# Performance work log

Hardware: AMD Instinct MI355X
Metric: run time of the kernel (lower is better)

## Reference

```python
import jax, jax.numpy as jnp
import numpy as np

EPS = 1e-15
B, N, F, K = 16, 1024, 512, 128  # graphs, max_nodes, feat dim, clusters


def setup_inputs() -> dict:
    key = jax.random.key(0)
    k0, k1, k2 = jax.random.split(key, 3)
    rng = np.random.default_rng(0)
    # Ragged graph sizes (between N/2 and N nodes per graph)
    counts = rng.integers(N // 2, N + 1, size=B)
    T = int(counts.sum())
    batch = np.repeat(np.arange(B), counts)
    starts = np.repeat(np.concatenate([[0], np.cumsum(counts)[:-1]]), counts)
    column = np.arange(T) - starts
    flat_index = batch * N + column  # as in _build_motifpool_dense_layout
    mask_flat = np.zeros(B * N, dtype=bool)
    mask_flat[flat_index] = True
    mask = mask_flat.reshape(B, N)
    x = jax.random.normal(k0, (T, F), dtype=jnp.float32)
    s = jax.random.normal(k1, (T, K), dtype=jnp.float32)
    a = jax.random.uniform(k2, (B, N, N), dtype=jnp.float32)
    m = jnp.asarray(mask)
    adj = (a + a.transpose(0, 2, 1)) * m[:, :, None] * m[:, None, :]
    return {
        'x': x,
        's': s,
        'adj': adj,
        'flat_index': jnp.asarray(flat_index, dtype=jnp.int32),
        'mask': m,
    }


def reference(x, s, adj, flat_index, mask):
    Bn, Nn = mask.shape
    Fd = x.shape[-1]
    Kd = s.shape[-1]
    # ragged -> dense scatter (index_copy_ equivalent)
    xd = jnp.zeros((Bn * Nn, Fd), x.dtype).at[flat_index].set(x).reshape(Bn, Nn, Fd)
    sd = jnp.zeros((Bn * Nn, Kd), s.dtype).at[flat_index].set(s).reshape(Bn, Nn, Kd)
    fmask = mask[..., None].astype(x.dtype)  # [B,N,1]
    sm = jax.nn.softmax(sd, axis=-1) * fmask
    xm = xd * fmask
    # pooled features and adjacency
    out = jnp.einsum('bnk,bnf->bkf', sm, xm)
    sa = jnp.einsum('bnk,bnm->bkm', sm, adj)
    out_adj = jnp.einsum('bkm,bml->bkl', sa, sm)
    # mincut loss: tr(S^T A S) / tr(S^T D S)
    mincut_num = jnp.trace(out_adj, axis1=-2, axis2=-1)
    d_flat = adj.sum(-1)  # node degrees [B,N]
    mincut_den = jnp.einsum('bn,bnk,bnk->b', d_flat, sm, sm)
    mincut_loss = jnp.mean(-(mincut_num / mincut_den))
    # orthogonality loss
    ss = jnp.einsum('bnk,bnl->bkl', sm, sm)
    ss_norm = jnp.linalg.norm(ss, axis=(-2, -1), keepdims=True)
    i_s = jnp.eye(Kd, dtype=ss.dtype)
    ortho_loss = jnp.mean(
        jnp.linalg.norm(ss / ss_norm - i_s / jnp.sqrt(jnp.asarray(Kd, ss.dtype)),
                        axis=(-2, -1)))
    # zero diagonal, symmetric degree-normalize
    eye_b = jnp.eye(Kd, dtype=bool)
    out_adj = jnp.where(eye_b, jnp.zeros((), out_adj.dtype), out_adj)
    d = jnp.sqrt(out_adj.sum(-1))[:, None, :] + EPS  # [B,1,K]
    out_adj = out_adj / d / d.transpose(0, 2, 1)
    return (sm, out, out_adj, mincut_loss, ortho_loss)
```

## Files before the change

kernel.cpp:

```cpp
#include <hip/hip_runtime.h>

constexpr int NB = 16, NN = 1024, NF = 512, NK = 128;
constexpr int NCH = 8;
constexpr int MSPLIT = 2;
constexpr float EPSV = 1e-15f;

typedef __attribute__((ext_vector_type(8))) short bf16x8;
typedef __attribute__((ext_vector_type(4))) float f32x4;

__device__ __forceinline__ f32x4 MFMA(bf16x8 a, bf16x8 b, f32x4 c) {
  return __builtin_amdgcn_mfma_f32_16x16x32_bf16(a, b, c, 0, 0, 0);
}

__device__ __forceinline__ unsigned short bf16_rn(float f) {
  unsigned int u = __float_as_uint(f);
  u += 0x7fffu + ((u >> 16) & 1u);
  return (unsigned short)(u >> 16);
}
__device__ __forceinline__ float bf16f(unsigned short h) {
  return __uint_as_float((unsigned int)h << 16);
}
__device__ __forceinline__ void split2(float f, unsigned short& h, unsigned short& lo) {
  h = bf16_rn(f);
  lo = bf16_rn(f - bf16f(h));
}

__global__ __launch_bounds__(256) void k_softmax(const float* __restrict__ s,
                                                 const int* __restrict__ fidx, int T,
                                                 float* __restrict__ sm,
                                                 unsigned short* __restrict__ smTh,
                                                 unsigned short* __restrict__ smTl,
                                                 int* __restrict__ rowof) {
  __shared__ float P[64][129];
  __shared__ int rof[64];
  int blk = blockIdx.x;
  int b = blk >> 4, n0 = (blk & 15) * 64;
  int tid = threadIdx.x, wv = tid >> 6, lane = tid & 63;
  if (tid < 64) {
    int d = b * NN + n0 + tid;
    int lo = 0, hi = T;
    while (lo < hi) {
      int mid = (lo + hi) >> 1;
      if (fidx[mid] < d) lo = mid + 1; else hi = mid;
    }
    int r = (lo < T && fidx[lo] == d) ? lo : -1;
    rof[tid] = r;
    rowof[d] = r;
  }
  __syncthreads();
  for (int i = 0; i < 16; ++i) {
    int r = wv * 16 + i;
    int ri = rof[r];
    float e0 = 0.f, e1 = 0.f;
    if (ri >= 0) {
      const float* row = s + (size_t)ri * NK;
      float a = row[lane], c = row[lane + 64];
      float m = fmaxf(a, c);
#pragma unroll
      for (int off = 32; off; off >>= 1) m = fmaxf(m, __shfl_xor(m, off, 64));
      e0 = expf(a - m);
      e1 = expf(c - m);
      float sum = e0 + e1;
#pragma unroll
      for (int off = 32; off; off >>= 1) sum += __shfl_xor(sum, off, 64);
      float inv = 1.0f / sum;
      e0 *= inv;
      e1 *= inv;
    }
    P[r][lane] = e0;
    P[r][lane + 64] = e1;
  }
  __syncthreads();
  int r2 = tid >> 2, cb = (tid & 3) * 32;
  float* orow = sm + ((size_t)b * NN + n0 + r2) * NK + cb;
#pragma unroll
  for (int j = 0; j < 8; ++j) {
    float4 v = make_float4(P[r2][cb + j * 4], P[r2][cb + j * 4 + 1],
                           P[r2][cb + j * 4 + 2], P[r2][cb + j * 4 + 3]);
    *(float4*)(orow + j * 4) = v;
  }
  for (int j = 0; j < 32; ++j) {
    int k = wv * 32 + j;
    float v = P[lane][k];
    unsigned short h, lo;
    split2(v, h, lo);
    size_t off = ((size_t)b * NK + k) * NN + n0 + lane;
    smTh[off] = h;
    smTl[off] = lo;
  }
}

__global__ __launch_bounds__(256) void k_adj_sm(const float* __restrict__ adj,
                                                const unsigned short* __restrict__ smTh,
                                                const unsigned short* __restrict__ smTl,
                                                float* __restrict__ Ytp,
                                                float* __restrict__ dfp) {
  __shared__ __align__(16) unsigned short STh[128][72], STl[128][72];
  __shared__ __align__(16) unsigned short ADh[64][72], ADl[64][72];
  int b = blockIdx.y, n0 = blockIdx.x * 64, z = blockIdx.z;
  int tid = threadIdx.x, wv = tid >> 6, l = tid & 63;
  int lr = l & 15, lk = l >> 4;
  int tk = tid >> 1, th = tid & 1;
  int sn = tid >> 2, sq = tid & 3;
  const float* A = adj + (size_t)b * NN * NN;
  f32x4 zero = {0.f, 0.f, 0.f, 0.f};
  f32x4 acc[2][4];
#pragma unroll
  for (int i = 0; i < 2; ++i)
#pragma unroll
    for (int j = 0; j < 4; ++j) acc[i][j] = zero;
  float rsacc = 0.f;
  for (int m0 = z * (NN / MSPLIT); m0 < (z + 1) * (NN / MSPLIT); m0 += 64) {
    __syncthreads();
    {
      const uint4* gh = (const uint4*)(smTh + ((size_t)b * NK + tk) * NN + m0 + th * 32);
      const uint4* gl = (const uint4*)(smTl + ((size_t)b * NK + tk) * NN + m0 + th * 32);
#pragma unroll
      for (int j = 0; j < 4; ++j) {
        *(uint4*)&STh[tk][th * 32 + j * 8] = gh[j];
        *(uint4*)&STl[tk][th * 32 + j * 8] = gl[j];
      }
    }
    {
      const float* ap = A + (size_t)(n0 + sn) * NN + m0 + sq * 16;
      float ps = 0.f;
#pragma unroll
      for (int j = 0; j < 4; ++j) {
        float4 v = *(const float4*)(ap + j * 4);
        ushort4 vh, vl;
        split2(v.x, vh.x, vl.x);
        split2(v.y, vh.y, vl.y);
        split2(v.z, vh.z, vl.z);
        split2(v.w, vh.w, vl.w);
        *(ushort4*)&ADh[sn][sq * 16 + j * 4] = vh;
        *(ushort4*)&ADl[sn][sq * 16 + j * 4] = vl;
        ps += v.x + v.y + v.z + v.w;
      }
      ps += __shfl_xor(ps, 1, 64);
      ps += __shfl_xor(ps, 2, 64);
      rsacc += ps;
    }
    __syncthreads();
#pragma unroll
    for (int s = 0; s < 2; ++s) {
      bf16x8 ah0 = *(const bf16x8*)&STh[wv * 32 + lr][s * 32 + lk * 8];
      bf16x8 ah1 = *(const bf16x8*)&STh[wv * 32 + 16 + lr][s * 32 + lk * 8];
      bf16x8 al0 = *(const bf16x8*)&STl[wv * 32 + lr][s * 32 + lk * 8];
      bf16x8 al1 = *(const bf16x8*)&STl[wv * 32 + 16 + lr][s * 32 + lk * 8];
#pragma unroll
      for (int nt = 0; nt < 4; ++nt) {
        bf16x8 bh = *(const bf16x8*)&ADh[nt * 16 + lr][s * 32 + lk * 8];
        bf16x8 bl = *(const bf16x8*)&ADl[nt * 16 + lr][s * 32 + lk * 8];
        acc[0][nt] = MFMA(ah0, bh, acc[0][nt]);
        acc[0][nt] = MFMA(ah0, bl, acc[0][nt]);
        acc[0][nt] = MFMA(al0, bh, acc[0][nt]);
        acc[1][nt] = MFMA(ah1, bh, acc[1][nt]);
        acc[1][nt] = MFMA(ah1, bl, acc[1][nt]);
        acc[1][nt] = MFMA(al1, bh, acc[1][nt]);
      }
    }
  }
  float* Yb = Ytp + ((size_t)z * NB + b) * NK * NN;
#pragma unroll
  for (int kt = 0; kt < 2; ++kt)
#pragma unroll
    for (int nt = 0; nt < 4; ++nt)
#pragma unroll
      for (int reg = 0; reg < 4; ++reg) {
        int k = wv * 32 + kt * 16 + lk * 4 + reg;
        int n = n0 + nt * 16 + lr;
        Yb[(size_t)k * NN + n] = acc[kt][nt][reg];
      }
  if (sq == 0) dfp[((size_t)z * NB + b) * NN + n0 + sn] = rsacc;
}

__global__ __launch_bounds__(512) void k_feat(const unsigned short* __restrict__ smTh,
                                              const unsigned short* __restrict__ smTl,
                                              const float* __restrict__ x,
                                              const int* __restrict__ rowof,
                                              float* __restrict__ outf) {
  __shared__ __align__(16) unsigned short STh[64][72], STl[64][72];
  __shared__ __align__(16) unsigned short XTh[64][72], XTl[64][72];
  int b = blockIdx.y, fbase = blockIdx.x * 64, kh = blockIdx.z * 64;
  int tid = threadIdx.x, wv = tid >> 6, l = tid & 63;
  int lr = l & 15, lk = l >> 4;
  int wk = (wv >> 1) * 16, wf = (wv & 1) * 32;
  int tk = tid >> 3, tq = tid & 7;
  f32x4 zero = {0.f, 0.f, 0.f, 0.f};
  f32x4 acc[2] = {zero, zero};
  for (int n0 = 0; n0 < NN; n0 += 64) {
    __syncthreads();
    {
      const uint4* gh = (const uint4*)(smTh + ((size_t)b * NK + kh + tk) * NN + n0 + tq * 8);
      const uint4* gl = (const uint4*)(smTl + ((size_t)b * NK + kh + tk) * NN + n0 + tq * 8);
      *(uint4*)&STh[tk][tq * 8] = gh[0];
      *(uint4*)&STl[tk][tq * 8] = gl[0];
    }
    {
      int ri = rowof[b * NN + n0 + tk];
      if (ri >= 0) {
        const float* xp = x + (size_t)ri * NF + fbase + tq * 8;
#pragma unroll
        for (int j = 0; j < 2; ++j) {
          float4 v = *(const float4*)(xp + j * 4);
          unsigned short h, lo;
          split2(v.x, h, lo); XTh[tq * 8 + j * 4 + 0][tk] = h; XTl[tq * 8 + j * 4 + 0][tk] = lo;
          split2(v.y, h, lo); XTh[tq * 8 + j * 4 + 1][tk] = h; XTl[tq * 8 + j * 4 + 1][tk] = lo;
          split2(v.z, h, lo); XTh[tq * 8 + j * 4 + 2][tk] = h; XTl[tq * 8 + j * 4 + 2][tk] = lo;
          split2(v.w, h, lo); XTh[tq * 8 + j * 4 + 3][tk] = h; XTl[tq * 8 + j * 4 + 3][tk] = lo;
        }
      } else {
#pragma unroll
        for (int e = 0; e < 8; ++e) {
          XTh[tq * 8 + e][tk] = 0;
          XTl[tq * 8 + e][tk] = 0;
        }
      }
    }
    __syncthreads();
#pragma unroll
    for (int s = 0; s < 2; ++s) {
      bf16x8 ah = *(const bf16x8*)&STh[wk + lr][s * 32 + lk * 8];
      bf16x8 al = *(const bf16x8*)&STl[wk + lr][s * 32 + lk * 8];
#pragma unroll
      for (int ft = 0; ft < 2; ++ft) {
        bf16x8 bh = *(const bf16x8*)&XTh[wf + ft * 16 + lr][s * 32 + lk * 8];
        bf16x8 bl = *(const bf16x8*)&XTl[wf + ft * 16 + lr][s * 32 + lk * 8];
        acc[ft] = MFMA(ah, bh, acc[ft]);
        acc[ft] = MFMA(ah, bl, acc[ft]);
        acc[ft] = MFMA(al, bh, acc[ft]);
      }
    }
  }
#pragma unroll
  for (int ft = 0; ft < 2; ++ft)
#pragma unroll
    for (int reg = 0; reg < 4; ++reg) {
      int kg = kh + wk + lk * 4 + reg;
      int fg = fbase + wf + ft * 16 + lr;
      outf[((size_t)b * NK + kg) * NF + fg] = acc[ft][reg];
    }
}

__global__ __launch_bounds__(256) void k_tt(const unsigned short* __restrict__ smTh,
                                            const unsigned short* __restrict__ smTl,
                                            const float* __restrict__ Ytp,
                                            const float* __restrict__ dfp,
                                            float* __restrict__ padj,
                                            float* __restrict__ pss,
                                            float* __restrict__ denp_arr) {
  __shared__ __align__(16) unsigned short STh[128][40], STl[128][40];
  __shared__ __align__(16) unsigned short YTh[128][40], YTl[128][40];
  __shared__ float red[256];
  int ch = blockIdx.x, b = blockIdx.y, z = blockIdx.z;
  int nbase = ch * 128;
  int tid = threadIdx.x, wv = tid >> 6, l = tid & 63;
  int lr = l & 15, lk = l >> 4;
  int tk = tid >> 1, th = tid & 1;
  f32x4 zero = {0.f, 0.f, 0.f, 0.f};
  f32x4 acc[2][8];
#pragma unroll
  for (int i = 0; i < 2; ++i)
#pragma unroll
    for (int j = 0; j < 8; ++j) acc[i][j] = zero;
  float denp = 0.f;
  for (int c = 0; c < 4; ++c) {
    int nn0 = nbase + c * 32;
    __syncthreads();
    {
      const unsigned short* gh = smTh + ((size_t)b * NK + tk) * NN + nn0 + th * 16;
      const unsigned short* gl = smTl + ((size_t)b * NK + tk) * NN + nn0 + th * 16;
#pragma unroll
      for (int j = 0; j < 4; ++j) {
        ushort4 hj = *(const ushort4*)(gh + j * 4);
        ushort4 lj = *(const ushort4*)(gl + j * 4);
        *(ushort4*)&STh[tk][th * 16 + j * 4] = hj;
        *(ushort4*)&STl[tk][th * 16 + j * 4] = lj;
        if (z) {
          float4 da = *(const float4*)(dfp + (size_t)b * NN + nn0 + th * 16 + j * 4);
          float4 db = *(const float4*)(dfp + (size_t)(NB + b) * NN + nn0 + th * 16 + j * 4);
          float v0 = bf16f(hj.x) + bf16f(lj.x), v1 = bf16f(hj.y) + bf16f(lj.y);
          float v2 = bf16f(hj.z) + bf16f(lj.z), v3 = bf16f(hj.w) + bf16f(lj.w);
          denp += (da.x + db.x) * v0 * v0 + (da.y + db.y) * v1 * v1 +
                  (da.z + db.z) * v2 * v2 + (da.w + db.w) * v3 * v3;
        }
      }
    }
    if (!z) {
      const float* y0 = Ytp + ((size_t)b * NK + tk) * NN + nn0 + th * 16;
      const float* y1 = y0 + (size_t)NB * NK * NN;
#pragma unroll
      for (int j = 0; j < 4; ++j) {
        float4 a = *(const float4*)(y0 + j * 4);
        float4 cc = *(const float4*)(y1 + j * 4);
        a.x += cc.x; a.y += cc.y; a.z += cc.z; a.w += cc.w;
        ushort4 vh, vl;
        split2(a.x, vh.x, vl.x);
        split2(a.y, vh.y, vl.y);
        split2(a.z, vh.z, vl.z);
        split2(a.w, vh.w, vl.w);
        *(ushort4*)&YTh[tk][th * 16 + j * 4] = vh;
        *(ushort4*)&YTl[tk][th * 16 + j * 4] = vl;
      }
    }
    __syncthreads();
    unsigned short(*Bh)[40] = z ? STh : YTh;
    unsigned short(*Bl)[40] = z ? STl : YTl;
    bf16x8 ah0 = *(const bf16x8*)&STh[wv * 32 + lr][lk * 8];
    bf16x8 ah1 = *(const bf16x8*)&STh[wv * 32 + 16 + lr][lk * 8];
    bf16x8 al0 = *(const bf16x8*)&STl[wv * 32 + lr][lk * 8];
    bf16x8 al1 = *(const bf16x8*)&STl[wv * 32 + 16 + lr][lk * 8];
#pragma unroll
    for (int ct = 0; ct < 8; ++ct) {
      bf16x8 bh = *(const bf16x8*)&Bh[ct * 16 + lr][lk * 8];
      bf16x8 bl = *(const bf16x8*)&Bl[ct * 16 + lr][lk * 8];
      acc[0][ct] = MFMA(ah0, bh, acc[0][ct]);
      acc[0][ct] = MFMA(ah0, bl, acc[0][ct]);
      acc[0][ct] = MFMA(al0, bh, acc[0][ct]);
      acc[1][ct] = MFMA(ah1, bh, acc[1][ct]);
      acc[1][ct] = MFMA(ah1, bl, acc[1][ct]);
      acc[1][ct] = MFMA(al1, bh, acc[1][ct]);
    }
  }
  float* O = (z ? pss : padj) + ((size_t)ch * NB + b) * NK * NK;
#pragma unroll
  for (int kt = 0; kt < 2; ++kt)
#pragma unroll
    for (int ct = 0; ct < 8; ++ct)
#pragma unroll
      for (int reg = 0; reg < 4; ++reg)
        O[(size_t)(wv * 32 + kt * 16 + lk * 4 + reg) * NK + ct * 16 + lr] =
            acc[kt][ct][reg];
  if (z) {
    red[tid] = denp;
    __syncthreads();
#pragma unroll
    for (int sft = 128; sft; sft >>= 1) {
      if (tid < sft) red[tid] += red[tid + sft];
      __syncthreads();
    }
    if (tid == 0) denp_arr[ch * NB + b] = red[0];
  }
}

__global__ __launch_bounds__(256) void k_reduce(const float* __restrict__ padj,
                                                const float* __restrict__ pss,
                                                float* __restrict__ adjraw,
                                                float* __restrict__ ssb) {
  size_t i = (size_t)blockIdx.x * 256 + threadIdx.x;
  size_t stride4 = (size_t)NB * NK * NK / 4;
  const float4* pa = (const float4*)padj + i;
  const float4* ps = (const float4*)pss + i;
  float4 a = make_float4(0.f, 0.f, 0.f, 0.f);
  float4 s = make_float4(0.f, 0.f, 0.f, 0.f);
#pragma unroll
  for (int ch = 0; ch < NCH; ++ch) {
    float4 va = pa[(size_t)ch * stride4];
    float4 vs = ps[(size_t)ch * stride4];
    a.x += va.x; a.y += va.y; a.z += va.z; a.w += va.w;
    s.x += vs.x; s.y += vs.y; s.z += vs.z; s.w += vs.w;
  }
  ((float4*)adjraw)[i] = a;
  ((float4*)ssb)[i] = s;
}

__device__ __forceinline__ float block_reduce_sum(float v, float* red) {
  int tid = threadIdx.x;
  red[tid] = v;
  __syncthreads();
#pragma unroll
  for (int sft = 128; sft; sft >>= 1) {
    if (tid < sft) red[tid] += red[tid + sft];
    __syncthreads();
  }
  float r = red[0];
  __syncthreads();
  return r;
}

__global__ __launch_bounds__(256) void k_finalize(const float* __restrict__ denp_arr,
                                                  const float* __restrict__ ssb,
                                                  float* __restrict__ out_adj,
                                                  float* __restrict__ out_loss) {
  __shared__ float red[256];
  __shared__ float sd[NK];
  int b = blockIdx.x, tid = threadIdx.x;
  float* AR = out_adj + (size_t)b * NK * NK;
  const float* SS = ssb + (size_t)b * NK * NK;

  float tv = (tid < NK) ? AR[tid * NK + tid] : 0.f;
  float trace = block_reduce_sum(tv, red);
  float den = 0.f;
#pragma unroll
  for (int ch = 0; ch < NCH; ++ch) den += denp_arr[ch * NB + b];

  float n2 = 0.f;
  for (int i4 = tid; i4 < NK * NK / 4; i4 += 256) {
    float4 v = *(const float4*)(SS + (size_t)i4 * 4);
    n2 += v.x * v.x + v.y * v.y + v.z * v.z + v.w * v.w;
  }
  float nrm = sqrtf(block_reduce_sum(n2, red));

  const float isk = 0.08838834764831845f;
  float osum = 0.f;
  for (int i = tid; i < NK * NK; i += 256) {
    int r = i >> 7, c = i & (NK - 1);
    float val = SS[i] / nrm - ((r == c) ? isk : 0.f);
    osum += val * val;
  }
  float ortho = sqrtf(block_reduce_sum(osum, red));

  if (tid < NK) {
    float rsumv = 0.f;
    const float* row = AR + (size_t)tid * NK;
    for (int j = 0; j < NK; ++j) rsumv += (j == tid) ? 0.f : row[j];
    sd[tid] = sqrtf(rsumv) + EPSV;
  }
  __syncthreads();

  for (int i = tid; i < NK * NK; i += 256) {
    int r = i >> 7, c = i & (NK - 1);
    AR[i] = (r == c) ? 0.f : AR[i] / (sd[r] * sd[c]);
  }

  if (tid == 0) {
    atomicAdd(&out_loss[0], -(trace / den) * (1.0f / NB));
    atomicAdd(&out_loss[1], ortho * (1.0f / NB));
  }
}

extern "C" void kernel_launch(void* const* d_in, const int* in_sizes, int n_in,
                              void* d_out, int out_size, void* d_ws, size_t ws_size,
                              hipStream_t stream) {
  const float* x = (const float*)d_in[0];
  const float* s = (const float*)d_in[1];
  const float* adj = (const float*)d_in[2];
  const int* fidx = (const int*)d_in[3];
  int T = in_sizes[3];

  float* out_sm = (float*)d_out;
  float* out_feat = out_sm + (size_t)NB * NN * NK;
  float* out_adj = out_feat + (size_t)NB * NK * NF;
  float* out_loss = out_adj + (size_t)NB * NK * NK;

  float* Ytp = (float*)d_ws;
  float* dfp = Ytp + (size_t)2 * NB * NK * NN;
  float* padj = dfp + (size_t)2 * NB * NN;
  float* pss = padj + (size_t)NCH * NB * NK * NK;
  float* ssb = pss + (size_t)NCH * NB * NK * NK;
  float* denp = ssb + (size_t)NB * NK * NK;
  unsigned short* smTh = (unsigned short*)(denp + NCH * NB);
  unsigned short* smTl = smTh + (size_t)NB * NK * NN;
  int* rowof = (int*)(smTl + (size_t)NB * NK * NN);

  hipMemsetAsync(out_loss, 0, 2 * sizeof(float), stream);

  k_softmax<<<NB * NN / 64, 256, 0, stream>>>(s, fidx, T, out_sm, smTh, smTl, rowof);
  k_adj_sm<<<dim3(NN / 64, NB, MSPLIT), 256, 0, stream>>>(adj, smTh, smTl, Ytp, dfp);
  k_feat<<<dim3(NF / 64, NB, 2), 512, 0, stream>>>(smTh, smTl, x, rowof, out_feat);
  k_tt<<<dim3(NCH, NB, 2), 256, 0, stream>>>(smTh, smTl, Ytp, dfp, padj, pss, denp);
  k_reduce<<<NB * NK * NK / 4 / 256, 256, 0, stream>>>(padj, pss, out_adj, ssb);
  k_finalize<<<NB, 256, 0, stream>>>(denp, ssb, out_adj, out_loss);
}
```

Measured before the change: 253.3 us.

## Pre-transpose x to bf16 in softmax kernel and drop its low-order split

```diff
diff --git a/kernel.cpp b/kernel.cpp
--- a/kernel.cpp
+++ b/kernel.cpp
@@ -26,34 +26,33 @@
 }
 
 __global__ __launch_bounds__(256) void k_softmax(const float* __restrict__ s,
+                                                 const float* __restrict__ x,
                                                  const int* __restrict__ fidx, int T,
                                                  float* __restrict__ sm,
                                                  unsigned short* __restrict__ smTh,
                                                  unsigned short* __restrict__ smTl,
-                                                 int* __restrict__ rowof) {
+                                                 unsigned short* __restrict__ xTh) {
   __shared__ float P[64][129];
-  __shared__ int rof[64];
+  __shared__ float XF[64][65];
+  __shared__ int sh_start, sh_cnt;
   int blk = blockIdx.x;
   int b = blk >> 4, n0 = (blk & 15) * 64;
   int tid = threadIdx.x, wv = tid >> 6, lane = tid & 63;
-  if (tid < 64) {
-    int d = b * NN + n0 + tid;
-    int lo = 0, hi = T;
-    while (lo < hi) {
-      int mid = (lo + hi) >> 1;
-      if (fidx[mid] < d) lo = mid + 1; else hi = mid;
-    }
-    int r = (lo < T && fidx[lo] == d) ? lo : -1;
-    rof[tid] = r;
-    rowof[d] = r;
+  if (tid == 0) {
+    int lo = 0, hi = T, tgt = b * NN;
+    while (lo < hi) { int m = (lo + hi) >> 1; if (fidx[m] < tgt) lo = m + 1; else hi = m; }
+    sh_start = lo;
+    int lo2 = lo, hi2 = T, tgt2 = b * NN + NN;
+    while (lo2 < hi2) { int m = (lo2 + hi2) >> 1; if (fidx[m] < tgt2) lo2 = m + 1; else hi2 = m; }
+    sh_cnt = lo2 - lo;
   }
   __syncthreads();
+  int start = sh_start, cnt = sh_cnt;
   for (int i = 0; i < 16; ++i) {
     int r = wv * 16 + i;
-    int ri = rof[r];
     float e0 = 0.f, e1 = 0.f;
-    if (ri >= 0) {
-      const float* row = s + (size_t)ri * NK;
+    if (n0 + r < cnt) {
+      const float* row = s + (size_t)(start + n0 + r) * NK;
       float a = row[lane], c = row[lane + 64];
       float m = fmaxf(a, c);
 #pragma unroll
@@ -87,6 +86,31 @@
     size_t off = ((size_t)b * NK + k) * NN + n0 + lane;
     smTh[off] = h;
     smTl[off] = lo;
+  }
+  int lrw = tid >> 2, f4 = tid & 3;
+  bool valid = (n0 + lrw) < cnt;
+  int gg = tid & 7;
+  for (int fc = 0; fc < 8; ++fc) {
+    __syncthreads();
+    const float* xp = x + (size_t)(start + n0 + lrw) * NF + fc * 64 + f4 * 16;
+#pragma unroll
+    for (int j = 0; j < 4; ++j) {
+      float4 v = valid ? *(const float4*)(xp + j * 4) : make_float4(0.f, 0.f, 0.f, 0.f);
+      XF[lrw][f4 * 16 + j * 4 + 0] = v.x;
+      XF[lrw][f4 * 16 + j * 4 + 1] = v.y;
+      XF[lrw][f4 * 16 + j * 4 + 2] = v.z;
+      XF[lrw][f4 * 16 + j * 4 + 3] = v.w;
+    }
+    __syncthreads();
+#pragma unroll
+    for (int p = 0; p < 2; ++p) {
+      int fl = p * 32 + (tid >> 3);
+      unsigned short hh[8];
+#pragma unroll
+      for (int e = 0; e < 8; ++e) hh[e] = bf16_rn(XF[gg * 8 + e][fl]);
+      size_t off = ((size_t)b * NF + fc * 64 + fl) * NN + n0 + gg * 8;
+      *(uint4*)(xTh + off) = *(uint4*)hh;
+    }
   }
 }
 
@@ -176,11 +200,10 @@
 
 __global__ __launch_bounds__(512) void k_feat(const unsigned short* __restrict__ smTh,
                                               const unsigned short* __restrict__ smTl,
-                                              const float* __restrict__ x,
-                                              const int* __restrict__ rowof,
+                                              const unsigned short* __restrict__ xTh,
                                               float* __restrict__ outf) {
   __shared__ __align__(16) unsigned short STh[64][72], STl[64][72];
-  __shared__ __align__(16) unsigned short XTh[64][72], XTl[64][72];
+  __shared__ __align__(16) unsigned short XT[64][72];
   int b = blockIdx.y, fbase = blockIdx.x * 64, kh = blockIdx.z * 64;
   int tid = threadIdx.x, wv = tid >> 6, l = tid & 63;
   int lr = l & 15, lk = l >> 4;
@@ -190,33 +213,11 @@
   f32x4 acc[2] = {zero, zero};
   for (int n0 = 0; n0 < NN; n0 += 64) {
     __syncthreads();
-    {
-      const uint4* gh = (const uint4*)(smTh + ((size_t)b * NK + kh + tk) * NN + n0 + tq * 8);
-      const uint4* gl = (const uint4*)(smTl + ((size_t)b * NK + kh + tk) * NN + n0 + tq * 8);
-      *(uint4*)&STh[tk][tq * 8] = gh[0];
-      *(uint4*)&STl[tk][tq * 8] = gl[0];
-    }
-    {
-      int ri = rowof[b * NN + n0 + tk];
-      if (ri >= 0) {
-        const float* xp = x + (size_t)ri * NF + fbase + tq * 8;
-#pragma unroll
-        for (int j = 0; j < 2; ++j) {
-          float4 v = *(const float4*)(xp + j * 4);
-          unsigned short h, lo;
-          split2(v.x, h, lo); XTh[tq * 8 + j * 4 + 0][tk] = h; XTl[tq * 8 + j * 4 + 0][tk] = lo;
-          split2(v.y, h, lo); XTh[tq * 8 + j * 4 + 1][tk] = h; XTl[tq * 8 + j * 4 + 1][tk] = lo;
-          split2(v.z, h, lo); XTh[tq * 8 + j * 4 + 2][tk] = h; XTl[tq * 8 + j * 4 + 2][tk] = lo;
-          split2(v.w, h, lo); XTh[tq * 8 + j * 4 + 3][tk] = h; XTl[tq * 8 + j * 4 + 3][tk] = lo;
-        }
-      } else {
-#pragma unroll
-        for (int e = 0; e < 8; ++e) {
-          XTh[tq * 8 + e][tk] = 0;
-          XTl[tq * 8 + e][tk] = 0;
-        }
-      }
-    }
+    size_t so = ((size_t)b * NK + kh + tk) * NN + n0 + tq * 8;
+    *(uint4*)&STh[tk][tq * 8] = *(const uint4*)(smTh + so);
+    *(uint4*)&STl[tk][tq * 8] = *(const uint4*)(smTl + so);
+    size_t xo = ((size_t)b * NF + fbase + tk) * NN + n0 + tq * 8;
+    *(uint4*)&XT[tk][tq * 8] = *(const uint4*)(xTh + xo);
     __syncthreads();
 #pragma unroll
     for (int s = 0; s < 2; ++s) {
@@ -224,10 +225,8 @@
       bf16x8 al = *(const bf16x8*)&STl[wk + lr][s * 32 + lk * 8];
 #pragma unroll
       for (int ft = 0; ft < 2; ++ft) {
-        bf16x8 bh = *(const bf16x8*)&XTh[wf + ft * 16 + lr][s * 32 + lk * 8];
-        bf16x8 bl = *(const bf16x8*)&XTl[wf + ft * 16 + lr][s * 32 + lk * 8];
+        bf16x8 bh = *(const bf16x8*)&XT[wf + ft * 16 + lr][s * 32 + lk * 8];
         acc[ft] = MFMA(ah, bh, acc[ft]);
-        acc[ft] = MFMA(ah, bl, acc[ft]);
         acc[ft] = MFMA(al, bh, acc[ft]);
       }
     }
@@ -346,7 +345,9 @@
 __global__ __launch_bounds__(256) void k_reduce(const float* __restrict__ padj,
                                                 const float* __restrict__ pss,
                                                 float* __restrict__ adjraw,
-                                                float* __restrict__ ssb) {
+                                                float* __restrict__ ssb,
+                                                float* __restrict__ out_loss) {
+  if (blockIdx.x == 0 && threadIdx.x < 2) out_loss[threadIdx.x] = 0.f;
   size_t i = (size_t)blockIdx.x * 256 + threadIdx.x;
   size_t stride4 = (size_t)NB * NK * NK / 4;
   const float4* pa = (const float4*)padj + i;
@@ -451,14 +452,12 @@
   float* denp = ssb + (size_t)NB * NK * NK;
   unsigned short* smTh = (unsigned short*)(denp + NCH * NB);
   unsigned short* smTl = smTh + (size_t)NB * NK * NN;
-  int* rowof = (int*)(smTl + (size_t)NB * NK * NN);
-
-  hipMemsetAsync(out_loss, 0, 2 * sizeof(float), stream);
-
-  k_softmax<<<NB * NN / 64, 256, 0, stream>>>(s, fidx, T, out_sm, smTh, smTl, rowof);
+  unsigned short* xTh = smTl + (size_t)NB * NK * NN;
+
+  k_softmax<<<NB * NN / 64, 256, 0, stream>>>(s, x, fidx, T, out_sm, smTh, smTl, xTh);
   k_adj_sm<<<dim3(NN / 64, NB, MSPLIT), 256, 0, stream>>>(adj, smTh, smTl, Ytp, dfp);
-  k_feat<<<dim3(NF / 64, NB, 2), 512, 0, stream>>>(smTh, smTl, x, rowof, out_feat);
+  k_feat<<<dim3(NF / 64, NB, 2), 512, 0, stream>>>(smTh, smTl, xTh, out_feat);
   k_tt<<<dim3(NCH, NB, 2), 256, 0, stream>>>(smTh, smTl, Ytp, dfp, padj, pss, denp);
-  k_reduce<<<NB * NK * NK / 4 / 256, 256, 0, stream>>>(padj, pss, out_adj, ssb);
+  k_reduce<<<NB * NK * NK / 4 / 256, 256, 0, stream>>>(padj, pss, out_adj, ssb, out_loss);
   k_finalize<<<NB, 256, 0, stream>>>(denp, ssb, out_adj, out_loss);
 }
```

Measured after the change: 240.6 us. 1.05x faster.
